# Performance work log

Hardware: AMD Instinct MI355X
Metric: run time of the kernel (lower is better)

The kernel has to match this reference:

```python
import jax, jax.numpy as jnp
import numpy as np
from jax import lax

B, N, W = 32, 512, 256
C = 16            # branch channels; D = 4*C = 64
Z = 8             # SAE latent
E = 8             # sensor embedding dim
HD = 16           # GAT head dim = max(8, 32//2)
GOUT = 32         # GAT out dim
TOPK = 20
RHO, EPS = 0.05, 1e-6
KS = [2, 3, 5, 7]


def _glorot(key, shape):
    fan_in, fan_out = shape[0], shape[-1]
    lim = jnp.sqrt(6.0 / (fan_in + fan_out))
    return jax.random.uniform(key, shape, jnp.float32, -lim, lim)


def setup_inputs() -> dict:
    key = jax.random.key(0)
    ks = jax.random.split(key, 32)
    inp = {"x": jax.random.normal(ks[0], (B, N, W), jnp.float32)}
    # MSTCN conv weights: torch Conv1d weight [C, 1, k], bias [C]
    for i, k in enumerate(KS):
        inp[f"conv_w{k}"] = jax.random.normal(ks[1 + i], (C, 1, k), jnp.float32) * (1.0 / np.sqrt(k))
        inp[f"conv_b{k}"] = jnp.zeros((C,), jnp.float32)
    inp["enc_w"] = _glorot(ks[6], (4 * C, Z));  inp["enc_b"] = jnp.zeros((Z,), jnp.float32)
    inp["dec_w"] = _glorot(ks[7], (Z, W));      inp["dec_b"] = jnp.zeros((W,), jnp.float32)
    inp["sensor_emb"] = _glorot(ks[8], (N, E))
    gin = Z + E
    inp["gat0_w"] = _glorot(ks[9], (gin, HD))
    inp["gat0_asrc"] = _glorot(ks[10], (1, HD))[0]
    inp["gat0_adst"] = _glorot(ks[11], (1, HD))[0]
    inp["gat1_w"] = _glorot(ks[12], (gin, HD))
    inp["gat1_asrc"] = _glorot(ks[13], (1, HD))[0]
    inp["gat1_adst"] = _glorot(ks[14], (1, HD))[0]
    inp["proj_w"] = _glorot(ks[15], (2 * HD, GOUT)); inp["proj_b"] = jnp.zeros((GOUT,), jnp.float32)
    inp["head_w"] = _glorot(ks[16], (GOUT, 1));      inp["head_b"] = jnp.zeros((1,), jnp.float32)
    return inp


def _mstcn(x, convs):
    # x: [B,N,W] -> node_feat [B,N,4C]
    b, n, w = x.shape
    xr = x.reshape(b * n, 1, w)
    feats = []
    for (cw, cb), k in zip(convs, KS):
        pl = (k - 1) // 2
        pr = (k - 1) - pl
        y = lax.conv_general_dilated(xr, cw, (1,), [(pl, pr)],
                                     dimension_numbers=("NCH", "OIH", "NCH"))
        y = y + cb[None, :, None]                 # [B*N, C, W]
        feats.append(y.mean(-1).reshape(b, n, C)) # time mean -> [B,N,C]
    return jnp.concatenate(feats, -1)


def _graph_learning(sensor_emb):
    # returns A [N,N]
    nrm = jnp.sqrt(jnp.sum(sensor_emb * sensor_emb, -1, keepdims=True))
    emb = sensor_emb / jnp.maximum(nrm, 1e-12)
    sim = (emb @ emb.T) / jnp.sqrt(jnp.float32(E))
    n = sim.shape[0]
    sim_ns = sim.at[jnp.diag_indices(n)].set(-jnp.inf)
    idx = lax.top_k(sim_ns, TOPK)[1]                       # [N, topk]
    mask = jnp.zeros_like(sim).at[jnp.arange(n)[:, None], idx].set(1.0)
    return jax.nn.relu(sim) * mask + jnp.eye(n, dtype=sim.dtype)


def _gat_head(x, a, w, a_src, a_dst):
    # x [B,N,F], a [N,N] -> [B,N,HD]; eval mode (dropout off)
    h = x @ w                                   # [B,N,HD]
    e_src = h @ a_src                           # [B,N]
    e_dst = h @ a_dst                           # [B,N]
    e = jax.nn.leaky_relu(e_src[:, :, None] + e_dst[:, None, :], 0.2)  # [B,N,N]
    e = jnp.where((a > 0)[None], e, -jnp.inf)
    alpha = jax.nn.softmax(e, axis=-1)
    return alpha @ h


def reference(x, conv_w2, conv_b2, conv_w3, conv_b3, conv_w5, conv_b5,
              conv_w7, conv_b7, enc_w, enc_b, dec_w, dec_b, sensor_emb,
              gat0_w, gat0_asrc, gat0_adst, gat1_w, gat1_asrc, gat1_adst,
              proj_w, proj_b, head_w, head_b):
    convs = [(conv_w2, conv_b2), (conv_w3, conv_b3), (conv_w5, conv_b5), (conv_w7, conv_b7)]
    node_feat = _mstcn(x, convs)                           # [B,N,64]
    # Sparse autoencoder
    z = node_feat @ enc_w + enc_b                          # [B,N,Z]
    recon = z @ dec_w + dec_b                              # [B,N,W]
    act = jax.nn.sigmoid(z)
    rho_hat = jnp.clip(act.mean((0, 1)), EPS, 1.0 - EPS)
    kl = jnp.sum(RHO * jnp.log(RHO / rho_hat) + (1.0 - RHO) * jnp.log((1.0 - RHO) / (1.0 - rho_hat)))
    sparsity_dev = jnp.mean(jnp.abs(act - RHO), -1)        # [B,N]
    # Graph learning + GAT
    a = _graph_learning(sensor_emb)                        # [N,N]
    e_b = jnp.broadcast_to(sensor_emb[None], (x.shape[0], N, E))
    gat_in = jnp.concatenate([z, e_b], -1)                 # [B,N,Z+E]
    h0 = _gat_head(gat_in, a, gat0_w, gat0_asrc, gat0_adst)
    h1 = _gat_head(gat_in, a, gat1_w, gat1_asrc, gat1_adst)
    h = jnp.concatenate([h0, h1], -1)
    fused = jax.nn.elu(h @ proj_w + proj_b)                # [B,N,GOUT]
    predicted = (fused @ head_w + head_b)[..., 0]          # [B,N]
    return predicted, recon, kl, sparsity_dev
```

## Files before the change

kernel.cpp:

```cpp
#include <hip/hip_runtime.h>
#include <math.h>

#define B_   32
#define N_   512
#define W_   256
#define BN_  (B_*N_)
#define NBLK_A 2048
#define RHOG   2048

__device__ __forceinline__ float wave_reduce_sum64(float v) {
#pragma unroll
    for (int m = 32; m >= 1; m >>= 1) v += __shfl_xor(v, m);
    return v;
}

__global__ __launch_bounds__(256) void kC2(
    const float* __restrict__ se,
    const float* __restrict__ w2, const float* __restrict__ b2,
    const float* __restrict__ w3, const float* __restrict__ b3,
    const float* __restrict__ w5, const float* __restrict__ b5,
    const float* __restrict__ w7, const float* __restrict__ b7,
    const float* __restrict__ enc_w, const float* __restrict__ enc_b,
    const float* __restrict__ g0w, const float* __restrict__ g0s, const float* __restrict__ g0d,
    const float* __restrict__ g1w, const float* __restrict__ g1s, const float* __restrict__ g1d,
    int* __restrict__ adj, float* __restrict__ ws_gam, float* __restrict__ ws_gsz,
    float* __restrict__ ws_gA)
{
    __shared__ float en[N_][9];
    __shared__ float sim[N_];
    __shared__ int   wc[8];

    const int tid = threadIdx.x;

    if (blockIdx.x == N_) {
        if (tid < 64) {
            const int zi = tid & 7, t = tid >> 3;
            float acc = (t == 7) ? enc_b[zi] : 0.f;
#define GAM_KI(KI, KK, CW, CB)                                                  \
            {                                                                   \
                const int k = KK; const int pl = (k - 1) >> 1;                  \
                _Pragma("unroll")                                               \
                for (int ch = 0; ch < 16; ++ch) {                               \
                    const int c = KI * 16 + ch; float a;                        \
                    if (t == 7) a = CB[ch];                                     \
                    else if (t == 0) {                                          \
                        a = 0.f;                                                \
                        _Pragma("unroll")                                       \
                        for (int j = 0; j < k; ++j) a += CW[ch*k+j];            \
                        a *= (1.f/(float)W_);                                   \
                    } else if (t <= 3) {                                        \
                        const int j = pl + t;                                   \
                        a = (j < k) ? -CW[ch*k+j]*(1.f/(float)W_) : 0.f;        \
                    } else {                                                    \
                        const int j = pl - (t - 3);                             \
                        a = (j >= 0) ? -CW[ch*k+j]*(1.f/(float)W_) : 0.f;       \
                    }                                                           \
                    acc += a * enc_w[c*8+zi];                                   \
                }                                                               \
            }
            GAM_KI(0, 2, w2, b2)
            GAM_KI(1, 3, w3, b3)
            GAM_KI(2, 5, w5, b5)
            GAM_KI(3, 7, w7, b7)
#undef GAM_KI
            ws_gam[zi*8+t] = acc;
        } else if (tid < 96) {
            const int q = (tid-64) >> 3, f = (tid-64) & 7;
            const float* gw = (q >> 1) ? g1w : g0w;
            const float* av = (q >> 1) ? ((q&1) ? g1d : g1s) : ((q&1) ? g0d : g0s);
            float v = 0.f;
#pragma unroll
            for (int d = 0; d < 16; ++d) v += gw[f*16+d] * av[d];
            ws_gsz[q*8+f] = v;
        } else if (tid < 128) {
            const int q = (tid-96) >> 3, f = (tid-96) & 7;
            const float* gw = (q >> 1) ? g1w : g0w;
            const float* av = (q >> 1) ? ((q&1) ? g1d : g1s) : ((q&1) ? g0d : g0s);
            float v = 0.f;
#pragma unroll
            for (int d = 0; d < 16; ++d) v += gw[(8+f)*16+d] * av[d];
            ws_gA[q*8+f] = v;
        }
        return;
    }

    const int i = blockIdx.x;

#pragma unroll
    for (int p = 0; p < 2; ++p) {
        const int rr = tid + p * 256;
        float v[8]; float ss = 0.f;
#pragma unroll
        for (int e = 0; e < 8; ++e) { v[e] = se[rr*8+e]; ss += v[e]*v[e]; }
        const float inv = 1.0f / fmaxf(sqrtf(ss), 1e-12f);
#pragma unroll
        for (int e = 0; e < 8; ++e) en[rr][e] = v[e] * inv;
    }
    __syncthreads();

    float ei[8];
#pragma unroll
    for (int e = 0; e < 8; ++e) ei[e] = en[i][e];
    const int j0 = tid, j1 = tid + 256;
    float s0 = 0.f, s1 = 0.f;
#pragma unroll
    for (int e = 0; e < 8; ++e) { s0 += ei[e]*en[j0][e]; s1 += ei[e]*en[j1][e]; }
    s0 *= 0.35355339059327373f;
    s1 *= 0.35355339059327373f;
    if (j0 == i) s0 = -3.4e38f;
    if (j1 == i) s1 = -3.4e38f;
    sim[j0] = s0; sim[j1] = s1;
    __syncthreads();

    int r0 = 0, r1 = 0;
    for (int q = 0; q < N_/4; ++q) {
        const float4 s4 = reinterpret_cast<const float4*>(sim)[q];
        const int jj = q * 4;
#pragma unroll
        for (int u = 0; u < 4; ++u) {
            const float sj = (u==0) ? s4.x : (u==1) ? s4.y : (u==2) ? s4.z : s4.w;
            r0 += (sj > s0 || (sj == s0 && (jj+u) < j0)) ? 1 : 0;
            r1 += (sj > s1 || (sj == s1 && (jj+u) < j1)) ? 1 : 0;
        }
    }
    const bool sel0 = (r0 < 20) && (s0 > 0.f);
    const bool sel1 = (r1 < 20) && (s1 > 0.f);

    const int wave = tid >> 6, lane = tid & 63;
    const unsigned long long m0 = __ballot(sel0);
    const unsigned long long m1 = __ballot(sel1);
    if (lane == 0) { wc[wave] = __popcll(m0); wc[4+wave] = __popcll(m1); }
    __syncthreads();
    int base0 = 1, base1 = 1;
#pragma unroll
    for (int w = 0; w < 4; ++w) base1 += wc[w];
    for (int w = 0; w < 4; ++w) {
        if (w < wave) { base0 += wc[w]; base1 += wc[4+w]; }
    }
    const unsigned long long below = (lane == 0) ? 0ull : (~0ull >> (64 - lane));
    if (sel0) adj[i*24 + 1 + base0 + __popcll(m0 & below)] = j0;
    if (sel1) adj[i*24 + 1 + base1 + __popcll(m1 & below)] = j1;
    if (tid == 0) {
        int cnt = 1;
#pragma unroll
        for (int w = 0; w < 8; ++w) cnt += wc[w];
        adj[i*24] = cnt;
        adj[i*24 + 1] = i;
    }
}

__global__ __launch_bounds__(256) void kA(
    const float* __restrict__ x,
    const float* __restrict__ dec_w, const float* __restrict__ dec_b,
    const float* __restrict__ g0w, const float* __restrict__ g1w,
    const float* __restrict__ se,
    const float* __restrict__ ws_gam, const float* __restrict__ ws_gsz,
    const float* __restrict__ ws_gA,
    float* __restrict__ out_recon, float* __restrict__ out_sdev,
    float* __restrict__ ws_h, float* __restrict__ ws_e, float* __restrict__ ws_rho)
{
    __shared__ float lds_rho[4][8];
    const int wave = threadIdx.x >> 6;
    const int lane = threadIdx.x & 63;
    const int r0 = (blockIdx.x << 3) + (wave << 1);
    const int n0 = r0 & (N_ - 1), n1 = (r0 + 1) & (N_ - 1);

    const float4 xv0 = reinterpret_cast<const float4*>(x)[(size_t)r0 * 64 + lane];
    const float4 xv1 = reinterpret_cast<const float4*>(x)[(size_t)(r0+1) * 64 + lane];
    const float4 ph0 = reinterpret_cast<const float4*>(x)[(size_t)r0 * 64];
    const float4 pt0 = reinterpret_cast<const float4*>(x)[(size_t)r0 * 64 + 63];
    const float4 ph1 = reinterpret_cast<const float4*>(x)[(size_t)(r0+1) * 64];
    const float4 pt1 = reinterpret_cast<const float4*>(x)[(size_t)(r0+1) * 64 + 63];

    float S0 = xv0.x + xv0.y + xv0.z + xv0.w;
    float S1 = xv1.x + xv1.y + xv1.z + xv1.w;
#pragma unroll
    for (int m = 32; m >= 1; m >>= 1) { S0 += __shfl_xor(S0, m); S1 += __shfl_xor(S1, m); }

    const float P10 = ph0.x, P20 = P10 + ph0.y, P30 = P20 + ph0.z;
    const float Q10 = pt0.w, Q20 = Q10 + pt0.z, Q30 = Q20 + pt0.y;
    const float P11 = ph1.x, P21 = P11 + ph1.y, P31 = P21 + ph1.z;
    const float Q11 = pt1.w, Q21 = Q11 + pt1.z, Q31 = Q21 + pt1.y;

    float z0[8], z1[8];
#pragma unroll
    for (int zi = 0; zi < 8; ++zi) {
        const float4 g0 = reinterpret_cast<const float4*>(ws_gam)[zi * 2];
        const float4 g1 = reinterpret_cast<const float4*>(ws_gam)[zi * 2 + 1];
        z0[zi] = g1.w + g0.x*S0 + g0.y*P10 + g0.z*P20 + g0.w*P30
                       + g1.x*Q10 + g1.y*Q20 + g1.z*Q30;
        z1[zi] = g1.w + g0.x*S1 + g0.y*P11 + g0.z*P21 + g0.w*P31
                       + g1.x*Q11 + g1.y*Q21 + g1.z*Q31;
    }

    {
        const float4 db = reinterpret_cast<const float4*>(dec_b)[lane];
        float4 rec0 = db, rec1 = db;
#pragma unroll
        for (int zi = 0; zi < 8; ++zi) {
            const float4 dw = reinterpret_cast<const float4*>(dec_w)[zi * 64 + lane];
            rec0.x += z0[zi]*dw.x; rec0.y += z0[zi]*dw.y; rec0.z += z0[zi]*dw.z; rec0.w += z0[zi]*dw.w;
            rec1.x += z1[zi]*dw.x; rec1.y += z1[zi]*dw.y; rec1.z += z1[zi]*dw.z; rec1.w += z1[zi]*dw.w;
        }
        reinterpret_cast<float4*>(out_recon)[(size_t)r0 * 64 + lane] = rec0;
        reinterpret_cast<float4*>(out_recon)[(size_t)(r0+1) * 64 + lane] = rec1;
    }

    if (lane < 16) {
        const int zi = lane & 7;
        const int rr = lane >> 3;
        float zl = 0.f;
#pragma unroll
        for (int p = 0; p < 8; ++p)
            zl = (zi == p) ? (rr ? z1[p] : z0[p]) : zl;
        const float a = 1.0f / (1.0f + __expf(-zl));
        float sd = fabsf(a - 0.05f);
        sd += __shfl_xor(sd, 1); sd += __shfl_xor(sd, 2); sd += __shfl_xor(sd, 4);
        if (zi == 0) out_sdev[r0 + rr] = sd * 0.125f;
        const float rho = a + __shfl_xor(a, 8);
        if (lane < 8) lds_rho[wave][lane] = rho;
    }

    if (lane < 32) {
        const float* gw = (lane >> 4) ? g1w : g0w;
        const int dd = lane & 15;
        float gwz[16];
#pragma unroll
        for (int f = 0; f < 16; ++f) gwz[f] = gw[f * 16 + dd];
        float h0 = 0.f, h1 = 0.f;
#pragma unroll
        for (int f = 0; f < 8; ++f) { h0 += z0[f] * gwz[f]; h1 += z1[f] * gwz[f]; }
#pragma unroll
        for (int f = 0; f < 8; ++f) {
            h0 += se[n0 * 8 + f] * gwz[8 + f];
            h1 += se[n1 * 8 + f] * gwz[8 + f];
        }
        ws_h[(size_t)r0 * 32 + lane] = h0;
        ws_h[(size_t)(r0+1) * 32 + lane] = h1;
    } else if (lane < 40) {
        const int q = (lane - 32) & 3;
        const int rr = (lane - 32) >> 2;
        const int nn = rr ? n1 : n0;
        float v = 0.f;
#pragma unroll
        for (int f = 0; f < 8; ++f) v += se[nn * 8 + f] * ws_gA[q * 8 + f];
#pragma unroll
        for (int f = 0; f < 8; ++f) v += (rr ? z1[f] : z0[f]) * ws_gsz[q * 8 + f];
        ws_e[(size_t)(r0 + rr) * 4 + q] = v;
    }

    __syncthreads();
    if (threadIdx.x < 8) {
        const float t = lds_rho[0][threadIdx.x] + lds_rho[1][threadIdx.x]
                      + lds_rho[2][threadIdx.x] + lds_rho[3][threadIdx.x];
        ws_rho[(size_t)blockIdx.x * 8 + threadIdx.x] = t;
    }
}

__global__ __launch_bounds__(256) void kD(
    const float* __restrict__ ws_h, const float* __restrict__ ws_e,
    const int* __restrict__ adj,
    const float* __restrict__ proj_w, const float* __restrict__ proj_b,
    const float* __restrict__ head_w, const float* __restrict__ head_b,
    float* __restrict__ out_pred,
    const float* __restrict__ ws_rho, float* __restrict__ out_kl)
{
    __shared__ float red[4][8];
    const int lane = threadIdx.x & 63;
    const int wave = threadIdx.x >> 6;
    const int half = lane >> 5;
    const int t32 = lane & 31;
    const int ri = (wave << 1) + half;
    const int r = (blockIdx.x << 3) + ri;
    const int b = r >> 9;
    const int i = r & (N_ - 1);
    const int cnt = adj[i * 24];

    const float4 er = reinterpret_cast<const float4*>(ws_e)[r];

    const int j = (t32 < cnt) ? adj[i * 24 + 1 + t32] : i;
    const int rj = (b << 9) | j;
    const float4 ejv = reinterpret_cast<const float4*>(ws_e)[rj];
    float e0 = er.x + ejv.y;  e0 = (e0 >= 0.f) ? e0 : 0.2f * e0;
    float e1 = er.z + ejv.w;  e1 = (e1 >= 0.f) ? e1 : 0.2f * e1;
    if (t32 >= cnt) { e0 = -3.4e38f; e1 = -3.4e38f; }
    float m0 = e0, m1 = e1;
#pragma unroll
    for (int m = 16; m >= 1; m >>= 1) {
        m0 = fmaxf(m0, __shfl_xor(m0, m));
        m1 = fmaxf(m1, __shfl_xor(m1, m));
    }
    float w0 = (t32 < cnt) ? __expf(e0 - m0) : 0.f;
    float w1 = (t32 < cnt) ? __expf(e1 - m1) : 0.f;
    float s0 = w0, s1 = w1;
#pragma unroll
    for (int m = 16; m >= 1; m >>= 1) {
        s0 += __shfl_xor(s0, m);
        s1 += __shfl_xor(s1, m);
    }

    const int d = t32;
    const int head = d >> 4;
    const float sinv = 1.0f / (head ? s1 : s0);
    float acc = 0.f;
#pragma unroll
    for (int t = 0; t < 21; ++t) {
        const float wt0 = __shfl(w0, t, 32);
        const float wt1 = __shfl(w1, t, 32);
        const int   jt  = __shfl(j, t, 32);
        const float wt  = head ? wt1 : wt0;
        acc += wt * ws_h[(size_t)((b << 9) | jt) * 32 + d];
    }
    const float hval = acc * sinv;

    float f = proj_b[d];
#pragma unroll
    for (int dd = 0; dd < 32; ++dd) {
        const float hv = __shfl(hval, dd, 32);
        f += hv * proj_w[dd * 32 + d];
    }
    f = (f > 0.f) ? f : expm1f(f);
    float p = f * head_w[d];
#pragma unroll
    for (int mm = 16; mm >= 1; mm >>= 1) p += __shfl_xor(p, mm);
    if (d == 0) out_pred[r] = p + head_b[0];

    if (blockIdx.x == 0) {
        float t8[8] = {0, 0, 0, 0, 0, 0, 0, 0};
        for (int g = (int)threadIdx.x; g < RHOG; g += 256) {
            const float4 a  = reinterpret_cast<const float4*>(ws_rho)[g * 2];
            const float4 bb = reinterpret_cast<const float4*>(ws_rho)[g * 2 + 1];
            t8[0] += a.x;  t8[1] += a.y;  t8[2] += a.z;  t8[3] += a.w;
            t8[4] += bb.x; t8[5] += bb.y; t8[6] += bb.z; t8[7] += bb.w;
        }
#pragma unroll
        for (int m = 32; m >= 1; m >>= 1)
#pragma unroll
            for (int zi = 0; zi < 8; ++zi) t8[zi] += __shfl_xor(t8[zi], m);
        if (lane == 0) {
#pragma unroll
            for (int zi = 0; zi < 8; ++zi) red[wave][zi] = t8[zi];
        }
        __syncthreads();
        if (threadIdx.x == 0) {
            float kl = 0.f;
#pragma unroll
            for (int zi = 0; zi < 8; ++zi) {
                float rh = (red[0][zi] + red[1][zi] + red[2][zi] + red[3][zi])
                           * (1.0f / (float)BN_);
                rh = fminf(fmaxf(rh, 1e-6f), 1.0f - 1e-6f);
                kl += 0.05f * logf(0.05f / rh) + 0.95f * logf(0.95f / (1.0f - rh));
            }
            out_kl[0] = kl;
        }
    }
}

extern "C" void kernel_launch(void* const* d_in, const int* in_sizes, int n_in,
                              void* d_out, int out_size, void* d_ws, size_t ws_size,
                              hipStream_t stream)
{
    (void)in_sizes; (void)n_in; (void)out_size; (void)ws_size;
    const float* x     = (const float*)d_in[0];
    const float* w2    = (const float*)d_in[1];
    const float* b2    = (const float*)d_in[2];
    const float* w3    = (const float*)d_in[3];
    const float* b3    = (const float*)d_in[4];
    const float* w5    = (const float*)d_in[5];
    const float* b5    = (const float*)d_in[6];
    const float* w7    = (const float*)d_in[7];
    const float* b7    = (const float*)d_in[8];
    const float* enc_w = (const float*)d_in[9];
    const float* enc_b = (const float*)d_in[10];
    const float* dec_w = (const float*)d_in[11];
    const float* dec_b = (const float*)d_in[12];
    const float* se    = (const float*)d_in[13];
    const float* g0w   = (const float*)d_in[14];
    const float* g0s   = (const float*)d_in[15];
    const float* g0d   = (const float*)d_in[16];
    const float* g1w   = (const float*)d_in[17];
    const float* g1s   = (const float*)d_in[18];
    const float* g1d   = (const float*)d_in[19];
    const float* pw    = (const float*)d_in[20];
    const float* pb    = (const float*)d_in[21];
    const float* hw    = (const float*)d_in[22];
    const float* hb    = (const float*)d_in[23];

    float* out       = (float*)d_out;
    float* out_pred  = out;
    float* out_recon = out + 16384;
    float* out_kl    = out + 16384 + 4194304;
    float* out_sdev  = out_kl + 1;

    float* ws_h   = (float*)d_ws;
    float* ws_e   = ws_h   + (size_t)BN_ * 32;
    float* ws_rho = ws_e   + (size_t)BN_ * 4;
    float* ws_gam = ws_rho + (size_t)RHOG * 8;
    float* ws_gsz = ws_gam + 64;
    float* ws_gA  = ws_gsz + 32;
    int*   ws_adj = (int*)(ws_gA + 32);

    hipLaunchKernelGGL(kC2, dim3(N_ + 1), dim3(256), 0, stream,
                       se, w2, b2, w3, b3, w5, b5, w7, b7, enc_w, enc_b,
                       g0w, g0s, g0d, g1w, g1s, g1d,
                       ws_adj, ws_gam, ws_gsz, ws_gA);
    hipLaunchKernelGGL(kA, dim3(NBLK_A), dim3(256), 0, stream,
                       x, dec_w, dec_b, g0w, g1w, se,
                       ws_gam, ws_gsz, ws_gA,
                       out_recon, out_sdev, ws_h, ws_e, ws_rho);
    hipLaunchKernelGGL(kD, dim3(BN_ / 8), dim3(256), 0, stream,
                       ws_h, ws_e, ws_adj, pw, pb, hw, hb, out_pred,
                       ws_rho, out_kl);
}
```

Baseline: 54.85 us.

## Split graph preprocessing into normalize kernel and wave-per-row iterative top-k

Sensor-embedding normalization now runs once in a small pre-kernel that writes to a workspace, instead of every one of the 512 blocks renormalizing all rows. The parameter folding moves into that kernel and stages its weights in LDS first. Top-k neighbor selection becomes one wavefront per row doing 20 rounds of shuffle-based argmax, replacing the O(N^2) rank counting per block. This adds an extra kernel launch and a serial dependency. The early break when the best similarity is non-positive mirrors the old rule of keeping only positive scores.

```diff
diff --git a/kernel.cpp b/kernel.cpp
--- a/kernel.cpp
+++ b/kernel.cpp
@@ -14,7 +14,7 @@
     return v;
 }
 
-__global__ __launch_bounds__(256) void kC2(
+__global__ __launch_bounds__(256) void kPre(
     const float* __restrict__ se,
     const float* __restrict__ w2, const float* __restrict__ b2,
     const float* __restrict__ w3, const float* __restrict__ b3,
@@ -23,130 +23,134 @@
     const float* __restrict__ enc_w, const float* __restrict__ enc_b,
     const float* __restrict__ g0w, const float* __restrict__ g0s, const float* __restrict__ g0d,
     const float* __restrict__ g1w, const float* __restrict__ g1s, const float* __restrict__ g1d,
-    int* __restrict__ adj, float* __restrict__ ws_gam, float* __restrict__ ws_gsz,
-    float* __restrict__ ws_gA)
+    float* __restrict__ en_g, float* __restrict__ ws_gam,
+    float* __restrict__ ws_gsz, float* __restrict__ ws_gA)
 {
-    __shared__ float en[N_][9];
-    __shared__ float sim[N_];
-    __shared__ int   wc[8];
-
     const int tid = threadIdx.x;
 
-    if (blockIdx.x == N_) {
-        if (tid < 64) {
-            const int zi = tid & 7, t = tid >> 3;
-            float acc = (t == 7) ? enc_b[zi] : 0.f;
-#define GAM_KI(KI, KK, CW, CB)                                                  \
-            {                                                                   \
-                const int k = KK; const int pl = (k - 1) >> 1;                  \
-                _Pragma("unroll")                                               \
-                for (int ch = 0; ch < 16; ++ch) {                               \
-                    const int c = KI * 16 + ch; float a;                        \
-                    if (t == 7) a = CB[ch];                                     \
-                    else if (t == 0) {                                          \
-                        a = 0.f;                                                \
-                        _Pragma("unroll")                                       \
-                        for (int j = 0; j < k; ++j) a += CW[ch*k+j];            \
-                        a *= (1.f/(float)W_);                                   \
-                    } else if (t <= 3) {                                        \
-                        const int j = pl + t;                                   \
-                        a = (j < k) ? -CW[ch*k+j]*(1.f/(float)W_) : 0.f;        \
-                    } else {                                                    \
-                        const int j = pl - (t - 3);                             \
-                        a = (j >= 0) ? -CW[ch*k+j]*(1.f/(float)W_) : 0.f;       \
-                    }                                                           \
-                    acc += a * enc_w[c*8+zi];                                   \
+    if (blockIdx.x == 0) {
+#pragma unroll
+        for (int p = 0; p < 2; ++p) {
+            const int rr = tid + p * 256;
+            const float4 a = reinterpret_cast<const float4*>(se)[rr * 2];
+            const float4 b = reinterpret_cast<const float4*>(se)[rr * 2 + 1];
+            const float ss = a.x*a.x + a.y*a.y + a.z*a.z + a.w*a.w
+                           + b.x*b.x + b.y*b.y + b.z*b.z + b.w*b.w;
+            const float inv = 1.0f / fmaxf(sqrtf(ss), 1e-12f);
+            float4 oa = a, ob = b;
+            oa.x*=inv; oa.y*=inv; oa.z*=inv; oa.w*=inv;
+            ob.x*=inv; ob.y*=inv; ob.z*=inv; ob.w*=inv;
+            reinterpret_cast<float4*>(en_g)[rr * 2]     = oa;
+            reinterpret_cast<float4*>(en_g)[rr * 2 + 1] = ob;
+        }
+        return;
+    }
+
+    __shared__ float L[1432];
+    const int oW2=0, oW3=32, oW5=80, oW7=160;
+    const int oB2=272, oB3=288, oB5=304, oB7=320;
+    const int oEW=336, oEB=848, oG0=856, oG1=1112, oAV=1368;
+#define CPY(off, src, n) for (int t = tid; t < (n); t += 256) L[(off)+t] = (src)[t];
+    CPY(oW2, w2, 32)  CPY(oW3, w3, 48)  CPY(oW5, w5, 80)  CPY(oW7, w7, 112)
+    CPY(oB2, b2, 16)  CPY(oB3, b3, 16)  CPY(oB5, b5, 16)  CPY(oB7, b7, 16)
+    CPY(oEW, enc_w, 512)  CPY(oEB, enc_b, 8)
+    CPY(oG0, g0w, 256)    CPY(oG1, g1w, 256)
+    CPY(oAV, g0s, 16) CPY(oAV+16, g0d, 16) CPY(oAV+32, g1s, 16) CPY(oAV+48, g1d, 16)
+#undef CPY
+    __syncthreads();
+
+    if (tid < 64) {
+        const int zi = tid & 7, t = tid >> 3;
+        float acc = (t == 7) ? L[oEB + zi] : 0.f;
+#define GAM_KI(BASE_C, OFFW, OFFB, KK)                                          \
+        {                                                                       \
+            const int k = KK; const int pl = (k - 1) >> 1;                      \
+            _Pragma("unroll")                                                   \
+            for (int ch = 0; ch < 16; ++ch) {                                   \
+                float a;                                                        \
+                if (t == 7) a = L[OFFB + ch];                                   \
+                else if (t == 0) {                                              \
+                    a = 0.f;                                                    \
+                    _Pragma("unroll")                                           \
+                    for (int j = 0; j < k; ++j) a += L[OFFW + ch*k + j];        \
+                    a *= (1.f/(float)W_);                                       \
+                } else if (t <= 3) {                                            \
+                    const int j = pl + t;                                       \
+                    a = (j < k) ? -L[OFFW + ch*k + j]*(1.f/(float)W_) : 0.f;    \
+                } else {                                                        \
+                    const int j = pl - (t - 3);                                 \
+                    a = (j >= 0) ? -L[OFFW + ch*k + j]*(1.f/(float)W_) : 0.f;   \
                 }                                                               \
-            }
-            GAM_KI(0, 2, w2, b2)
-            GAM_KI(1, 3, w3, b3)
-            GAM_KI(2, 5, w5, b5)
-            GAM_KI(3, 7, w7, b7)
+                acc += a * L[oEW + (BASE_C + ch)*8 + zi];                       \
+            }                                                                   \
+        }
+        GAM_KI(0,  oW2, oB2, 2)
+        GAM_KI(16, oW3, oB3, 3)
+        GAM_KI(32, oW5, oB5, 5)
+        GAM_KI(48, oW7, oB7, 7)
 #undef GAM_KI
-            ws_gam[zi*8+t] = acc;
-        } else if (tid < 96) {
-            const int q = (tid-64) >> 3, f = (tid-64) & 7;
-            const float* gw = (q >> 1) ? g1w : g0w;
-            const float* av = (q >> 1) ? ((q&1) ? g1d : g1s) : ((q&1) ? g0d : g0s);
-            float v = 0.f;
-#pragma unroll
-            for (int d = 0; d < 16; ++d) v += gw[f*16+d] * av[d];
-            ws_gsz[q*8+f] = v;
-        } else if (tid < 128) {
-            const int q = (tid-96) >> 3, f = (tid-96) & 7;
-            const float* gw = (q >> 1) ? g1w : g0w;
-            const float* av = (q >> 1) ? ((q&1) ? g1d : g1s) : ((q&1) ? g0d : g0s);
-            float v = 0.f;
-#pragma unroll
-            for (int d = 0; d < 16; ++d) v += gw[(8+f)*16+d] * av[d];
-            ws_gA[q*8+f] = v;
-        }
-        return;
-    }
-
-    const int i = blockIdx.x;
-
-#pragma unroll
-    for (int p = 0; p < 2; ++p) {
-        const int rr = tid + p * 256;
-        float v[8]; float ss = 0.f;
-#pragma unroll
-        for (int e = 0; e < 8; ++e) { v[e] = se[rr*8+e]; ss += v[e]*v[e]; }
-        const float inv = 1.0f / fmaxf(sqrtf(ss), 1e-12f);
-#pragma unroll
-        for (int e = 0; e < 8; ++e) en[rr][e] = v[e] * inv;
-    }
-    __syncthreads();
-
-    float ei[8];
-#pragma unroll
-    for (int e = 0; e < 8; ++e) ei[e] = en[i][e];
-    const int j0 = tid, j1 = tid + 256;
-    float s0 = 0.f, s1 = 0.f;
-#pragma unroll
-    for (int e = 0; e < 8; ++e) { s0 += ei[e]*en[j0][e]; s1 += ei[e]*en[j1][e]; }
-    s0 *= 0.35355339059327373f;
-    s1 *= 0.35355339059327373f;
-    if (j0 == i) s0 = -3.4e38f;
-    if (j1 == i) s1 = -3.4e38f;
-    sim[j0] = s0; sim[j1] = s1;
-    __syncthreads();
-
-    int r0 = 0, r1 = 0;
-    for (int q = 0; q < N_/4; ++q) {
-        const float4 s4 = reinterpret_cast<const float4*>(sim)[q];
-        const int jj = q * 4;
-#pragma unroll
-        for (int u = 0; u < 4; ++u) {
-            const float sj = (u==0) ? s4.x : (u==1) ? s4.y : (u==2) ? s4.z : s4.w;
-            r0 += (sj > s0 || (sj == s0 && (jj+u) < j0)) ? 1 : 0;
-            r1 += (sj > s1 || (sj == s1 && (jj+u) < j1)) ? 1 : 0;
-        }
-    }
-    const bool sel0 = (r0 < 20) && (s0 > 0.f);
-    const bool sel1 = (r1 < 20) && (s1 > 0.f);
-
-    const int wave = tid >> 6, lane = tid & 63;
-    const unsigned long long m0 = __ballot(sel0);
-    const unsigned long long m1 = __ballot(sel1);
-    if (lane == 0) { wc[wave] = __popcll(m0); wc[4+wave] = __popcll(m1); }
-    __syncthreads();
-    int base0 = 1, base1 = 1;
-#pragma unroll
-    for (int w = 0; w < 4; ++w) base1 += wc[w];
-    for (int w = 0; w < 4; ++w) {
-        if (w < wave) { base0 += wc[w]; base1 += wc[4+w]; }
-    }
-    const unsigned long long below = (lane == 0) ? 0ull : (~0ull >> (64 - lane));
-    if (sel0) adj[i*24 + 1 + base0 + __popcll(m0 & below)] = j0;
-    if (sel1) adj[i*24 + 1 + base1 + __popcll(m1 & below)] = j1;
-    if (tid == 0) {
-        int cnt = 1;
-#pragma unroll
-        for (int w = 0; w < 8; ++w) cnt += wc[w];
-        adj[i*24] = cnt;
-        adj[i*24 + 1] = i;
-    }
+        ws_gam[zi*8+t] = acc;
+    } else if (tid < 96) {
+        const int q = (tid-64) >> 3, f = (tid-64) & 7;
+        const int gw = (q >> 1) ? oG1 : oG0;
+        const int av = oAV + q*16;
+        float v = 0.f;
+#pragma unroll
+        for (int d = 0; d < 16; ++d) v += L[gw + f*16+d] * L[av + d];
+        ws_gsz[q*8+f] = v;
+    } else if (tid < 128) {
+        const int q = (tid-96) >> 3, f = (tid-96) & 7;
+        const int gw = (q >> 1) ? oG1 : oG0;
+        const int av = oAV + q*16;
+        float v = 0.f;
+#pragma unroll
+        for (int d = 0; d < 16; ++d) v += L[gw + (8+f)*16+d] * L[av + d];
+        ws_gA[q*8+f] = v;
+    }
+}
+
+__global__ __launch_bounds__(256) void kTop(const float* __restrict__ en_g,
+                                            int* __restrict__ adj)
+{
+    const int wave = threadIdx.x >> 6;
+    const int lane = threadIdx.x & 63;
+    const int i = (blockIdx.x << 2) + wave;
+
+    const float4 ei0 = reinterpret_cast<const float4*>(en_g)[i * 2];
+    const float4 ei1 = reinterpret_cast<const float4*>(en_g)[i * 2 + 1];
+
+    float v[8];
+#pragma unroll
+    for (int q = 0; q < 8; ++q) {
+        const int j = (q << 6) + lane;
+        const float4 a = reinterpret_cast<const float4*>(en_g)[j * 2];
+        const float4 b = reinterpret_cast<const float4*>(en_g)[j * 2 + 1];
+        const float d = ei0.x*a.x + ei0.y*a.y + ei0.z*a.z + ei0.w*a.w
+                      + ei1.x*b.x + ei1.y*b.y + ei1.z*b.z + ei1.w*b.w;
+        v[q] = (j == i) ? -3.4e38f : d * 0.35355339059327373f;
+    }
+
+    int cnt = 1;
+    if (lane == 0) adj[i * 24 + 1] = i;
+    for (int it = 0; it < 20; ++it) {
+        float bv = v[0]; int bq = 0;
+#pragma unroll
+        for (int q = 1; q < 8; ++q) if (v[q] > bv) { bv = v[q]; bq = q; }
+        int bj = (bq << 6) + lane;
+#pragma unroll
+        for (int m = 32; m >= 1; m >>= 1) {
+            const float ov = __shfl_xor(bv, m);
+            const int   oj = __shfl_xor(bj, m);
+            if (ov > bv || (ov == bv && oj < bj)) { bv = ov; bj = oj; }
+        }
+        if (bv <= 0.f) break;
+        if (lane == 0) adj[i * 24 + 1 + cnt] = bj;
+        cnt++;
+        const int wq = bj >> 6, wl = bj & 63;
+#pragma unroll
+        for (int q = 0; q < 8; ++q) if (q == wq && lane == wl) v[q] = -3.4e38f;
+    }
+    if (lane == 0) adj[i * 24] = cnt;
 }
 
 __global__ __launch_bounds__(256) void kA(
@@ -398,12 +402,14 @@
     float* ws_gam = ws_rho + (size_t)RHOG * 8;
     float* ws_gsz = ws_gam + 64;
     float* ws_gA  = ws_gsz + 32;
-    int*   ws_adj = (int*)(ws_gA + 32);
-
-    hipLaunchKernelGGL(kC2, dim3(N_ + 1), dim3(256), 0, stream,
+    float* ws_en  = ws_gA  + 32;
+    int*   ws_adj = (int*)(ws_en + (size_t)N_ * 8);
+
+    hipLaunchKernelGGL(kPre, dim3(2), dim3(256), 0, stream,
                        se, w2, b2, w3, b3, w5, b5, w7, b7, enc_w, enc_b,
                        g0w, g0s, g0d, g1w, g1s, g1d,
-                       ws_adj, ws_gam, ws_gsz, ws_gA);
+                       ws_en, ws_gam, ws_gsz, ws_gA);
+    hipLaunchKernelGGL(kTop, dim3(N_ / 4), dim3(256), 0, stream, ws_en, ws_adj);
     hipLaunchKernelGGL(kA, dim3(NBLK_A), dim3(256), 0, stream,
                        x, dec_w, dec_b, g0w, g1w, se,
                        ws_gam, ws_gsz, ws_gA,
```

Measured after the change: 58.87 us. 7.3% more time.

## Replace rank-count top-k with per-wave iterative argmax selection

Applied to the files above, without the earlier changes.

Graph-learning top-k now assigns one wave per sensor row instead of one 256-thread block, and normalizes embeddings on the fly rather than staging all normalized embeddings in LDS. The O(N) rank-counting per element is replaced by 20 rounds of a wave-wide shuffle argmax with early exit once the best similarity is non-positive. This removes LDS traffic, block barriers and the quadratic comparison work, shrinking the grid from 513 to 129 blocks. Edge ordering changes to descending similarity, and each thread recomputes norms redundantly.

```diff
diff --git a/kernel.cpp b/kernel.cpp
--- a/kernel.cpp
+++ b/kernel.cpp
@@ -6,15 +6,10 @@
 #define W_   256
 #define BN_  (B_*N_)
 #define NBLK_A 2048
+#define NBLK_T 128
 #define RHOG   2048
 
-__device__ __forceinline__ float wave_reduce_sum64(float v) {
-#pragma unroll
-    for (int m = 32; m >= 1; m >>= 1) v += __shfl_xor(v, m);
-    return v;
-}
-
-__global__ __launch_bounds__(256) void kC2(
+__global__ __launch_bounds__(256) void kST(
     const float* __restrict__ se,
     const float* __restrict__ w2, const float* __restrict__ b2,
     const float* __restrict__ w3, const float* __restrict__ b3,
@@ -26,13 +21,11 @@
     int* __restrict__ adj, float* __restrict__ ws_gam, float* __restrict__ ws_gsz,
     float* __restrict__ ws_gA)
 {
-    __shared__ float en[N_][9];
-    __shared__ float sim[N_];
-    __shared__ int   wc[8];
-
-    const int tid = threadIdx.x;
-
-    if (blockIdx.x == N_) {
+    const int tid  = threadIdx.x;
+    const int wave = tid >> 6;
+    const int lane = tid & 63;
+
+    if (blockIdx.x == NBLK_T) {
         if (tid < 64) {
             const int zi = tid & 7, t = tid >> 3;
             float acc = (t == 7) ? enc_b[zi] : 0.f;
@@ -84,69 +77,48 @@
         return;
     }
 
-    const int i = blockIdx.x;
-
-#pragma unroll
-    for (int p = 0; p < 2; ++p) {
-        const int rr = tid + p * 256;
-        float v[8]; float ss = 0.f;
-#pragma unroll
-        for (int e = 0; e < 8; ++e) { v[e] = se[rr*8+e]; ss += v[e]*v[e]; }
-        const float inv = 1.0f / fmaxf(sqrtf(ss), 1e-12f);
-#pragma unroll
-        for (int e = 0; e < 8; ++e) en[rr][e] = v[e] * inv;
-    }
-    __syncthreads();
-
-    float ei[8];
-#pragma unroll
-    for (int e = 0; e < 8; ++e) ei[e] = en[i][e];
-    const int j0 = tid, j1 = tid + 256;
-    float s0 = 0.f, s1 = 0.f;
-#pragma unroll
-    for (int e = 0; e < 8; ++e) { s0 += ei[e]*en[j0][e]; s1 += ei[e]*en[j1][e]; }
-    s0 *= 0.35355339059327373f;
-    s1 *= 0.35355339059327373f;
-    if (j0 == i) s0 = -3.4e38f;
-    if (j1 == i) s1 = -3.4e38f;
-    sim[j0] = s0; sim[j1] = s1;
-    __syncthreads();
-
-    int r0 = 0, r1 = 0;
-    for (int q = 0; q < N_/4; ++q) {
-        const float4 s4 = reinterpret_cast<const float4*>(sim)[q];
-        const int jj = q * 4;
-#pragma unroll
-        for (int u = 0; u < 4; ++u) {
-            const float sj = (u==0) ? s4.x : (u==1) ? s4.y : (u==2) ? s4.z : s4.w;
-            r0 += (sj > s0 || (sj == s0 && (jj+u) < j0)) ? 1 : 0;
-            r1 += (sj > s1 || (sj == s1 && (jj+u) < j1)) ? 1 : 0;
-        }
-    }
-    const bool sel0 = (r0 < 20) && (s0 > 0.f);
-    const bool sel1 = (r1 < 20) && (s1 > 0.f);
-
-    const int wave = tid >> 6, lane = tid & 63;
-    const unsigned long long m0 = __ballot(sel0);
-    const unsigned long long m1 = __ballot(sel1);
-    if (lane == 0) { wc[wave] = __popcll(m0); wc[4+wave] = __popcll(m1); }
-    __syncthreads();
-    int base0 = 1, base1 = 1;
-#pragma unroll
-    for (int w = 0; w < 4; ++w) base1 += wc[w];
-    for (int w = 0; w < 4; ++w) {
-        if (w < wave) { base0 += wc[w]; base1 += wc[4+w]; }
-    }
-    const unsigned long long below = (lane == 0) ? 0ull : (~0ull >> (64 - lane));
-    if (sel0) adj[i*24 + 1 + base0 + __popcll(m0 & below)] = j0;
-    if (sel1) adj[i*24 + 1 + base1 + __popcll(m1 & below)] = j1;
-    if (tid == 0) {
-        int cnt = 1;
-#pragma unroll
-        for (int w = 0; w < 8; ++w) cnt += wc[w];
-        adj[i*24] = cnt;
-        adj[i*24 + 1] = i;
-    }
+    const int i = (blockIdx.x << 2) + wave;
+    const float4 a_i = reinterpret_cast<const float4*>(se)[i * 2];
+    const float4 b_i = reinterpret_cast<const float4*>(se)[i * 2 + 1];
+    const float ssi = a_i.x*a_i.x + a_i.y*a_i.y + a_i.z*a_i.z + a_i.w*a_i.w
+                    + b_i.x*b_i.x + b_i.y*b_i.y + b_i.z*b_i.z + b_i.w*b_i.w;
+    const float inv_i = 1.0f / fmaxf(sqrtf(ssi), 1e-12f);
+
+    float v[8];
+#pragma unroll
+    for (int q = 0; q < 8; ++q) {
+        const int j = (q << 6) + lane;
+        const float4 a = reinterpret_cast<const float4*>(se)[j * 2];
+        const float4 b = reinterpret_cast<const float4*>(se)[j * 2 + 1];
+        const float d = a_i.x*a.x + a_i.y*a.y + a_i.z*a.z + a_i.w*a.w
+                      + b_i.x*b.x + b_i.y*b.y + b_i.z*b.z + b_i.w*b.w;
+        const float ssj = a.x*a.x + a.y*a.y + a.z*a.z + a.w*a.w
+                        + b.x*b.x + b.y*b.y + b.z*b.z + b.w*b.w;
+        const float inv_j = 1.0f / fmaxf(sqrtf(ssj), 1e-12f);
+        v[q] = (j == i) ? -3.4e38f
+                        : d * inv_i * inv_j * 0.35355339059327373f;
+    }
+    int cnt = 1;
+    if (lane == 0) adj[i * 24 + 1] = i;
+    for (int it = 0; it < 20; ++it) {
+        float bv = v[0]; int bq = 0;
+#pragma unroll
+        for (int q = 1; q < 8; ++q) if (v[q] > bv) { bv = v[q]; bq = q; }
+        int bj = (bq << 6) + lane;
+#pragma unroll
+        for (int m = 32; m >= 1; m >>= 1) {
+            const float ov = __shfl_xor(bv, m);
+            const int   oj = __shfl_xor(bj, m);
+            if (ov > bv || (ov == bv && oj < bj)) { bv = ov; bj = oj; }
+        }
+        if (bv <= 0.f) break;
+        if (lane == 0) adj[i * 24 + 1 + cnt] = bj;
+        cnt++;
+        const int wq = bj >> 6, wl = bj & 63;
+#pragma unroll
+        for (int q = 0; q < 8; ++q) if (q == wq && lane == wl) v[q] = -3.4e38f;
+    }
+    if (lane == 0) adj[i * 24] = cnt;
 }
 
 __global__ __launch_bounds__(256) void kA(
@@ -400,7 +372,7 @@
     float* ws_gA  = ws_gsz + 32;
     int*   ws_adj = (int*)(ws_gA + 32);
 
-    hipLaunchKernelGGL(kC2, dim3(N_ + 1), dim3(256), 0, stream,
+    hipLaunchKernelGGL(kST, dim3(NBLK_T + 1), dim3(256), 0, stream,
                        se, w2, b2, w3, b3, w5, b5, w7, b7, enc_w, enc_b,
                        g0w, g0s, g0d, g1w, g1s, g1d,
                        ws_adj, ws_gam, ws_gsz, ws_gA);
```

Measured after the change: 48.58 us. 11.4% less time.
